# Kernel optimization log

Hardware: AMD Instinct MI355X
Metric: run time of the kernel (lower is better)

Reference implementation:

```python
import jax, jax.numpy as jnp
import numpy as np

T, B, OBS, H, GH = 512, 256, 512, 256, 256  # time, batch, obs_dim, FC_DIM_SIZE(=GRU hidden), GRU_HIDDEN_DIM (actor width)
ADIMS = (32, 32, 16, 64)
BIG = 1e10


def setup_inputs():
    key = jax.random.key(0)
    ks = jax.random.split(key, 16)
    f = lambda i, shp: (jax.random.normal(ks[i], shp, jnp.float32) / np.float32(np.sqrt(shp[0])))
    inp = {
        "hidden": jnp.zeros((B, H), jnp.float32),
        "obs": jax.random.normal(ks[0], (T, B, OBS), jnp.float32),
        "dones": jax.random.randint(ks[1], (T, B), 0, 2).astype(jnp.int32),
        "avail_lc1": jax.random.randint(ks[2], (T, B, ADIMS[0]), 0, 2).astype(jnp.int32),
        "avail_lc2": jax.random.randint(ks[3], (T, B, ADIMS[1]), 0, 2).astype(jnp.int32),
        "avail_mc": jax.random.randint(ks[4], (T, B, ADIMS[2]), 0, 2).astype(jnp.int32),
        "avail_hint": jax.random.randint(ks[5], (T, B, ADIMS[3]), 0, 2).astype(jnp.int32),
        "W_emb": f(6, (OBS, H)), "b_emb": jnp.zeros((H,), jnp.float32),
        "Wi": f(7, (H, 3 * H)), "bi": jnp.zeros((3 * H,), jnp.float32),
        "Wh": f(8, (H, 3 * H)), "bhn": jnp.zeros((H,), jnp.float32),
        "W_a": f(9, (H, GH)), "b_a": jnp.zeros((GH,), jnp.float32),
        "W_lc1": f(10, (GH, ADIMS[0])), "b_lc1": jnp.zeros((ADIMS[0],), jnp.float32),
        "W_lc2": f(11, (GH, ADIMS[1])), "b_lc2": jnp.zeros((ADIMS[1],), jnp.float32),
        "W_mc": f(12, (GH, ADIMS[2])), "b_mc": jnp.zeros((ADIMS[2],), jnp.float32),
        "W_hint": f(13, (GH, ADIMS[3])), "b_hint": jnp.zeros((ADIMS[3],), jnp.float32),
        "W_c1": f(14, (H, H)), "b_c1": jnp.zeros((H,), jnp.float32),
        "W_c2": f(15, (H, 1)), "b_c2": jnp.zeros((1,), jnp.float32),
    }
    return inp


def _gru_scan(hidden, emb, dones, Wi, bi, Wh, bhn):
    # flax GRUCell math: r=sig(ir+hr), z=sig(iz+hz), n=tanh(in + r*(hn+bhn)), h'=(1-z)*n + z*h
    def step(h, xt):
        e, d = xt  # e: [B,H], d: [B]
        h = jnp.where(d[:, None] != 0, jnp.zeros_like(h), h)  # per-step reset to zero carry
        gi = e @ Wi + bi   # [B,3H]
        gh = h @ Wh        # [B,3H]
        ir, iz, inn = jnp.split(gi, 3, axis=-1)
        hr, hz, hn = jnp.split(gh, 3, axis=-1)
        r = jax.nn.sigmoid(ir + hr)
        z = jax.nn.sigmoid(iz + hz)
        n = jnp.tanh(inn + r * (hn + bhn))
        nh = (1.0 - z) * n + z * h
        return nh, nh
    return jax.lax.scan(step, hidden, (emb, dones))


def reference(hidden, obs, dones, avail_lc1, avail_lc2, avail_mc, avail_hint,
              W_emb, b_emb, Wi, bi, Wh, bhn, W_a, b_a,
              W_lc1, b_lc1, W_lc2, b_lc2, W_mc, b_mc, W_hint, b_hint,
              W_c1, b_c1, W_c2, b_c2):
    emb = jax.nn.relu(obs @ W_emb + b_emb)                    # [T,B,H]
    hidden, y = _gru_scan(hidden, emb, dones, Wi, bi, Wh, bhn)  # y: [T,B,H]
    a = jax.nn.relu(y @ W_a + b_a)                            # [T,B,GH]
    mask = lambda logits, avail: logits - (1.0 - avail.astype(logits.dtype)) * BIG
    l_lc1 = mask(a @ W_lc1 + b_lc1, avail_lc1)
    l_lc2 = mask(a @ W_lc2 + b_lc2, avail_lc2)
    l_mc = mask(a @ W_mc + b_mc, avail_mc)
    l_hint = mask(a @ W_hint + b_hint, avail_hint)
    c = jax.nn.relu(y @ W_c1 + b_c1)                          # [T,B,H]
    critic = jnp.squeeze(c @ W_c2 + b_c2, axis=-1)            # [T,B]
    return (hidden, l_lc1, l_lc2, l_mc, l_hint, critic)
```

## Files before the change

kernel.cpp:

```cpp
#include <hip/hip_runtime.h>
#include <stdint.h>


typedef short short8 __attribute__((ext_vector_type(8)));
typedef float f32x4  __attribute__((ext_vector_type(4)));

#define T_DIM 512
#define CHUNK 32
#define NCH   16
#define GIPL  ((size_t)33554432)

#define OUT_HID  ((size_t)0)
#define OUT_LC1  ((size_t)65536)
#define OUT_LC2  ((size_t)4259840)
#define OUT_MC   ((size_t)8454144)
#define OUT_HINT ((size_t)10551296)
#define OUT_CRIT ((size_t)18939904)

__device__ __forceinline__ unsigned short f2bf(float f) {
    unsigned u = __float_as_uint(f);
    u += 0x7fffu + ((u >> 16) & 1u);
    return (unsigned short)(u >> 16);
}
__device__ __forceinline__ float bf2f(unsigned short h) {
    return __uint_as_float(((unsigned)h) << 16);
}

__device__ __forceinline__ unsigned short gru_cell(
    float ir, float iz, float inn, float ho,
    float hrv, float hzv, float hnv, float bh)
{
    float rg = 1.f / (1.f + __expf(-(ir + hrv)));
    float z  = 1.f / (1.f + __expf(-(iz + hzv)));
    float ex = __expf(2.f * (inn + rg * (hnv + bh)));
    float n  = 1.f - 2.f / (ex + 1.f);
    return f2bf((1.f - z) * n + z * ho);
}

__global__ __launch_bounds__(256, 4) void k_prep(
    const float* __restrict__ W_emb, const float* __restrict__ Wi,
    const float* __restrict__ Wh,    const float* __restrict__ W_a,
    const float* __restrict__ W_c1,  const float* __restrict__ W_lc1,
    const float* __restrict__ W_lc2, const float* __restrict__ W_mc,
    const float* __restrict__ W_hint,
    const float* __restrict__ b_lc1, const float* __restrict__ b_lc2,
    const float* __restrict__ b_mc,  const float* __restrict__ b_hint,
    unsigned short* __restrict__ WembF, unsigned short* __restrict__ WiF,
    unsigned short* __restrict__ WhF,   unsigned short* __restrict__ WacF,
    unsigned short* __restrict__ WlogF, float* __restrict__ blog,
    int* __restrict__ fixflag)
{
    int i = blockIdx.x * 256 + threadIdx.x;
    if (i < 131072) {
        int jj = i & 7, L = (i >> 3) & 63, kt32 = (i >> 9) & 15;
        int j = (i >> 13) & 3, q = (i >> 15) & 3;
        int n = q * 64 + j * 16 + (L & 15);
        int k = kt32 * 32 + ((L >> 4) << 3) + jj;
        WembF[i] = f2bf(W_emb[k * 256 + n]);
        return;
    }
    i -= 131072;
    if (i < 196608) {
        int jj = i & 7, L = (i >> 3) & 63, kk32 = (i >> 9) & 7;
        int j = (i >> 12) & 3, q = (i >> 14) & 3, nc = i >> 16;
        int n = nc * 256 + q * 64 + j * 16 + (L & 15);
        int k = kk32 * 32 + ((L >> 4) << 3) + jj;
        WiF[i] = f2bf(Wi[k * 768 + n]);
        return;
    }
    i -= 196608;
    if (i < 196608) {
        int jj = i & 7, L = (i >> 3) & 63, ks = (i >> 9) & 7, rest = i >> 12;
        int w = rest / 6, i6 = rest % 6, rho = i6 >> 1, s = i6 & 1;
        int k   = ks * 32 + ((L >> 4) << 3) + jj;
        int col = rho * 256 + w * 32 + s * 16 + (L & 15);
        WhF[i] = f2bf(Wh[k * 768 + col]);
        return;
    }
    i -= 196608;
    if (i < 131072) {
        int jj = i & 7, L = (i >> 3) & 63, kk32 = (i >> 9) & 7;
        int j = (i >> 12) & 3, q = (i >> 14) & 3, nc = (i >> 16) & 1;
        int n = nc * 256 + q * 64 + j * 16 + (L & 15);
        int k = kk32 * 32 + ((L >> 4) << 3) + jj;
        WacF[i] = f2bf(n < 256 ? W_a[k * 256 + n] : W_c1[k * 256 + (n - 256)]);
        return;
    }
    i -= 131072;
    if (i < 40960) {
        int jj = i & 7, L = (i >> 3) & 63, kk32 = (i >> 9) & 7;
        int j = i >> 12;
        int n = j * 16 + (L & 15);
        int k = kk32 * 32 + ((L >> 4) << 3) + jj;
        float v;
        if      (n < 32)  v = W_lc1[k * 32 + n];
        else if (n < 64)  v = W_lc2[k * 32 + (n - 32)];
        else if (n < 80)  v = W_mc [k * 16 + (n - 64)];
        else if (n < 144) v = W_hint[k * 64 + (n - 80)];
        else              v = 0.f;
        WlogF[i] = f2bf(v);
        return;
    }
    i -= 40960;
    if (i < 160) {
        float v;
        if      (i < 32)  v = b_lc1[i];
        else if (i < 64)  v = b_lc2[i - 32];
        else if (i < 80)  v = b_mc [i - 64];
        else if (i < 144) v = b_hint[i - 80];
        else              v = 0.f;
        blog[i] = v;
        return;
    }
    i -= 160;
    if (i == 0) *fixflag = 0;
}

__global__ __launch_bounds__(512, 3) void k_fused_g12(
    const float* __restrict__ obs, const unsigned short* __restrict__ WembF,
    const float* __restrict__ b_emb, const unsigned short* __restrict__ WiF,
    const float* __restrict__ bi, unsigned short* __restrict__ out)
{
    __shared__ unsigned short As[64][72];
    __shared__ unsigned short eS[64][264];
    const int tid = threadIdx.x, w = tid >> 6, L = tid & 63;
    const int mq = (w >> 2) * 32, wq = w & 3, nq = wq * 64;
    const int m0 = blockIdx.x * 64;
    const int lc = L & 15, lq8 = (L >> 4) * 8, lr = (L >> 4) * 4;
    const int sra = tid >> 3, sha = (tid & 7) * 8;

    f32x4 acc[2][4];
#pragma unroll
    for (int i = 0; i < 2; i++)
#pragma unroll
        for (int j = 0; j < 4; j++) acc[i][j] = 0;

    const float* Ag = obs + (size_t)(m0 + sra) * 512 + sha;
    for (int kt = 0; kt < 512; kt += 64) {
        {
            f32x4 v0 = *(const f32x4*)(Ag + kt);
            f32x4 v1 = *(const f32x4*)(Ag + kt + 4);
            short8 pk;
            pk[0] = (short)f2bf(v0[0]); pk[1] = (short)f2bf(v0[1]);
            pk[2] = (short)f2bf(v0[2]); pk[3] = (short)f2bf(v0[3]);
            pk[4] = (short)f2bf(v1[0]); pk[5] = (short)f2bf(v1[1]);
            pk[6] = (short)f2bf(v1[2]); pk[7] = (short)f2bf(v1[3]);
            *(short8*)&As[sra][sha] = pk;
        }
        __syncthreads();
#pragma unroll
        for (int ks = 0; ks < 2; ks++) {
            const int kt32 = (kt >> 5) + ks;
            short8 a[2], b[4];
#pragma unroll
            for (int i = 0; i < 2; i++)
                a[i] = *(const short8*)&As[mq + i * 16 + lc][ks * 32 + lq8];
#pragma unroll
            for (int j = 0; j < 4; j++)
                b[j] = *(const short8*)(WembF +
                        ((((size_t)(wq * 4 + j) * 16 + kt32) * 64 + L) * 8));
#pragma unroll
            for (int i = 0; i < 2; i++)
#pragma unroll
                for (int j = 0; j < 4; j++)
                    acc[i][j] = __builtin_amdgcn_mfma_f32_16x16x32_bf16(a[i], b[j], acc[i][j], 0, 0, 0);
        }
        __syncthreads();
    }
#pragma unroll
    for (int i = 0; i < 2; i++)
#pragma unroll
        for (int j = 0; j < 4; j++) {
            int col = nq + j * 16 + lc;
            float bv = b_emb[col];
#pragma unroll
            for (int rg = 0; rg < 4; rg++) {
                int row = mq + i * 16 + lr + rg;
                eS[row][col] = f2bf(fmaxf(acc[i][j][rg] + bv, 0.f));
            }
        }
    __syncthreads();

    for (int nc = 0; nc < 3; nc++) {
#pragma unroll
        for (int i = 0; i < 2; i++)
#pragma unroll
            for (int j = 0; j < 4; j++) acc[i][j] = 0;

#pragma unroll 2
        for (int kk = 0; kk < 256; kk += 32) {
            const int kk32 = kk >> 5;
            short8 a[2], b[4];
#pragma unroll
            for (int i = 0; i < 2; i++)
                a[i] = *(const short8*)&eS[mq + i * 16 + lc][kk + lq8];
#pragma unroll
            for (int j = 0; j < 4; j++)
                b[j] = *(const short8*)(WiF +
                        ((((size_t)((nc * 4 + wq) * 4 + j) * 8 + kk32) * 64 + L) * 8));
#pragma unroll
            for (int i = 0; i < 2; i++)
#pragma unroll
                for (int j = 0; j < 4; j++)
                    acc[i][j] = __builtin_amdgcn_mfma_f32_16x16x32_bf16(a[i], b[j], acc[i][j], 0, 0, 0);
        }
#pragma unroll
        for (int i = 0; i < 2; i++) {
            const int row0  = m0 + mq + i * 16 + lr;
            const int t     = row0 >> 8;
            const int g     = (row0 >> 4) & 15;
            const int rowg2 = (row0 >> 2) & 3;
#pragma unroll
            for (int jh = 0; jh < 2; jh++) {
                const int colb = nc * 256 + nq + jh * 32;
                const int gate = colb >> 8;
                const int w2   = (colb & 255) >> 5;
                short8 pk;
#pragma unroll
                for (int rg = 0; rg < 4; rg++)
#pragma unroll
                    for (int s = 0; s < 2; s++) {
                        int col = colb + s * 16 + lc;
                        float v = acc[i][jh * 2 + s][rg] + bi[col];
                        pk[rg * 2 + s] = (short)f2bf(v);
                    }
                size_t dst = (size_t)gate * GIPL +
                             (((size_t)(t * 16 + g) * 512) + (size_t)w2 * 64 +
                              (size_t)rowg2 * 16 + lc) * 8;
                *(short8*)(out + dst) = pk;
            }
        }
    }
}

__global__ __launch_bounds__(512, 3) void k_gemm_ac(
    const unsigned short* __restrict__ y, const unsigned short* __restrict__ WacF,
    const float* __restrict__ b_a, const float* __restrict__ b_c1,
    unsigned short* __restrict__ out)
{
    __shared__ unsigned short yS[64][264];
    const int tid = threadIdx.x, w = tid >> 6, L = tid & 63;
    const int mq = (w >> 2) * 32, wq = w & 3, nq = wq * 64;
    const int m0 = blockIdx.x * 64;
    const int lc = L & 15, lq8 = (L >> 4) * 8, lr = (L >> 4) * 4;

    {
        int r = tid >> 3, cb = (tid & 7) * 32;
        const unsigned short* yg = y + (size_t)(m0 + r) * 256 + cb;
#pragma unroll
        for (int c = 0; c < 32; c += 8)
            *(short8*)&yS[r][cb + c] = *(const short8*)(yg + c);
    }
    __syncthreads();

    for (int nc = 0; nc < 2; nc++) {
        f32x4 acc[2][4];
#pragma unroll
        for (int i = 0; i < 2; i++)
#pragma unroll
            for (int j = 0; j < 4; j++) acc[i][j] = 0;

#pragma unroll 2
        for (int kk = 0; kk < 256; kk += 32) {
            const int kk32 = kk >> 5;
            short8 a[2], b[4];
#pragma unroll
            for (int i = 0; i < 2; i++)
                a[i] = *(const short8*)&yS[mq + i * 16 + lc][kk + lq8];
#pragma unroll
            for (int j = 0; j < 4; j++)
                b[j] = *(const short8*)(WacF +
                        ((((size_t)((nc * 4 + wq) * 4 + j) * 8 + kk32) * 64 + L) * 8));
#pragma unroll
            for (int i = 0; i < 2; i++)
#pragma unroll
                for (int j = 0; j < 4; j++)
                    acc[i][j] = __builtin_amdgcn_mfma_f32_16x16x32_bf16(a[i], b[j], acc[i][j], 0, 0, 0);
        }
#pragma unroll
        for (int i = 0; i < 2; i++)
#pragma unroll
            for (int j = 0; j < 4; j++) {
                int col = nc * 256 + nq + j * 16 + lc;
                float bv = (col < 256) ? b_a[col] : b_c1[col - 256];
#pragma unroll
                for (int rg = 0; rg < 4; rg++) {
                    int row = m0 + mq + i * 16 + lr + rg;
                    out[(size_t)row * 512 + col] = f2bf(fmaxf(acc[i][j][rg] + bv, 0.f));
                }
            }
    }
}

__global__ __launch_bounds__(512, 1) void k_gru_main(
    const unsigned short* __restrict__ gi, const unsigned short* __restrict__ WhF,
    const int* __restrict__ dones, const float* __restrict__ h0,
    const float* __restrict__ bhn, unsigned short* __restrict__ y,
    unsigned short* __restrict__ hend)
{
    __shared__ unsigned short hT[2][16][264];
    __shared__ unsigned short yS[2][16][256];
    __shared__ unsigned int rowbits[16];
    const int tid = threadIdx.x, w = tid >> 6, L = tid & 63;
    const int g = blockIdx.x & 15, c = blockIdx.x >> 4;
    const int b0 = g * 16, t0 = c * CHUNK;
    const int rowg = L >> 4, lc = L & 15;

    short8 Bf[6][8];
#pragma unroll
    for (int i6 = 0; i6 < 6; i6++)
#pragma unroll
        for (int ks = 0; ks < 8; ks++)
            Bf[i6][ks] = *(const short8*)(WhF + ((((size_t)w * 6 + i6) * 8 + ks) * 64 + L) * 8);

    const float bh0 = bhn[w * 32 + lc], bh1 = bhn[w * 32 + 16 + lc];

    if (tid < 16) rowbits[tid] = 0;
    __syncthreads();
    {
        int tp = tid >> 4, r = tid & 15;
        if (dones[(t0 + tp) * 256 + b0 + r]) atomicOr(&rowbits[r], 1u << tp);
    }
    __syncthreads();

    unsigned rbr[4];
#pragma unroll
    for (int r = 0; r < 4; r++) rbr[r] = rowbits[rowg * 4 + r];

    {
        int hrow = tid >> 5, hcol = (tid & 31) * 8;
        bool rz = (rowbits[hrow] & 1u) != 0;
#pragma unroll
        for (int cc = 0; cc < 8; cc++) {
            unsigned short v = 0;
            if (c == 0 && !rz) v = f2bf(h0[(b0 + hrow) * 256 + hcol + cc]);
            hT[0][hrow][hcol + cc] = v;
        }
    }
    __syncthreads();

    const size_t gstep = (size_t)16 * 512 * 8;
    size_t gb = ((size_t)(t0 * 16 + g) * 512 + tid) * 8;
    short8 vir = *(const short8*)(gi + gb);
    short8 viz = *(const short8*)(gi + GIPL + gb);
    short8 vin = *(const short8*)(gi + 2 * GIPL + gb);

#pragma unroll 2
    for (int tp = 0; tp < CHUNK; tp++) {
        const int cur = tp & 1, nxt = cur ^ 1;
        const int t = t0 + tp;

        short8 nir, niz, nin;
        if (tp + 1 < CHUNK) {
            size_t gn = gb + (size_t)(tp + 1) * gstep;
            nir = *(const short8*)(gi + gn);
            niz = *(const short8*)(gi + GIPL + gn);
            nin = *(const short8*)(gi + 2 * GIPL + gn);
        }

        f32x4 acc0 = 0, acc1 = 0, acc2 = 0, acc3 = 0, acc4 = 0, acc5 = 0;
#pragma unroll
        for (int ks = 0; ks < 8; ks++) {
            short8 a = *(const short8*)&hT[cur][lc][ks * 32 + rowg * 8];
            acc0 = __builtin_amdgcn_mfma_f32_16x16x32_bf16(a, Bf[0][ks], acc0, 0, 0, 0);
            acc1 = __builtin_amdgcn_mfma_f32_16x16x32_bf16(a, Bf[1][ks], acc1, 0, 0, 0);
            acc2 = __builtin_amdgcn_mfma_f32_16x16x32_bf16(a, Bf[2][ks], acc2, 0, 0, 0);
            acc3 = __builtin_amdgcn_mfma_f32_16x16x32_bf16(a, Bf[3][ks], acc3, 0, 0, 0);
            acc4 = __builtin_amdgcn_mfma_f32_16x16x32_bf16(a, Bf[4][ks], acc4, 0, 0, 0);
            acc5 = __builtin_amdgcn_mfma_f32_16x16x32_bf16(a, Bf[5][ks], acc5, 0, 0, 0);
        }

#pragma unroll
        for (int s = 0; s < 2; s++) {
            const int j = w * 32 + s * 16 + lc;
            f32x4 hrv = s ? acc1 : acc0;
            f32x4 hzv = s ? acc3 : acc2;
            f32x4 hnv = s ? acc5 : acc4;
            float bh = s ? bh1 : bh0;
#pragma unroll
            for (int r = 0; r < 4; r++) {
                int row = rowg * 4 + r;
                float ir  = bf2f((unsigned short)vir[r * 2 + s]);
                float iz  = bf2f((unsigned short)viz[r * 2 + s]);
                float inn = bf2f((unsigned short)vin[r * 2 + s]);
                float ho  = bf2f(hT[cur][row][j]);
                unsigned short hb = gru_cell(ir, iz, inn, ho, hrv[r], hzv[r], hnv[r], bh);
                yS[cur][row][j] = hb;
                unsigned short hw = hb;
                if (tp + 1 < CHUNK && ((rbr[r] >> (tp + 1)) & 1u)) hw = 0;
                hT[nxt][row][j] = hw;
            }
        }
        __syncthreads();

        {
            int yrow = tid >> 5, ycol = (tid & 31) * 8;
            short8 yv = *(const short8*)&yS[cur][yrow][ycol];
            *(short8*)(y + ((size_t)t * 256 + b0 + yrow) * 256 + ycol) = yv;
            if (tp == CHUNK - 1)
                *(short8*)(hend + ((size_t)c * 256 + b0 + yrow) * 256 + ycol) = yv;
        }

        vir = nir; viz = niz; vin = nin;
    }
}

__global__ __launch_bounds__(512, 1) void k_gru_fix_par(
    const unsigned short* __restrict__ gi, const unsigned short* __restrict__ WhF,
    const int* __restrict__ dones, const float* __restrict__ bhn,
    const unsigned short* __restrict__ hend, unsigned short* __restrict__ y,
    int* __restrict__ flag)
{
    __shared__ unsigned short hT[2][16][264];
    __shared__ unsigned int rowbits[16], prevbits[16];
    __shared__ int sh_fd[16];
    const int tid = threadIdx.x, w = tid >> 6, L = tid & 63;
    const int g = blockIdx.x & 15, c = (blockIdx.x >> 4) + 1;
    const int b0 = g * 16, t0 = c * CHUNK;
    const int rowg = L >> 4, lc = L & 15;
    const int hrow = tid >> 5, hcol = (tid & 31) * 8;

    short8 Bf[6][8];
#pragma unroll
    for (int i6 = 0; i6 < 6; i6++)
#pragma unroll
        for (int ks = 0; ks < 8; ks++)
            Bf[i6][ks] = *(const short8*)(WhF + ((((size_t)w * 6 + i6) * 8 + ks) * 64 + L) * 8);

    const float bh0 = bhn[w * 32 + lc], bh1 = bhn[w * 32 + 16 + lc];

    if (tid < 16) { rowbits[tid] = 0; prevbits[tid] = 0; }
    __syncthreads();
    {
        int tp = tid >> 4, r = tid & 15;
        if (dones[(t0 + tp) * 256 + b0 + r])         atomicOr(&rowbits[r],  1u << tp);
        if (dones[(t0 - CHUNK + tp) * 256 + b0 + r]) atomicOr(&prevbits[r], 1u << tp);
    }
    __syncthreads();
    if (tid < 16) {
        unsigned m = rowbits[tid];
        sh_fd[tid] = m ? __builtin_ctz(m) : CHUNK;
        if (prevbits[tid] == 0) atomicOr(flag, 1);
    }
    __syncthreads();

    int maxfix = 0;
    unsigned rbr[4]; int fdr[4];
#pragma unroll
    for (int r = 0; r < 16; r++) maxfix = max(maxfix, sh_fd[r]);
    if (maxfix == 0) return;
#pragma unroll
    for (int r = 0; r < 4; r++) {
        rbr[r] = rowbits[rowg * 4 + r];
        fdr[r] = sh_fd[rowg * 4 + r];
    }

    {
        short8 hv = *(const short8*)(hend + ((size_t)(c - 1) * 256 + b0 + hrow) * 256 + hcol);
        if (rowbits[hrow] & 1u) { short8 z = {0,0,0,0,0,0,0,0}; hv = z; }
        *(short8*)&hT[0][hrow][hcol] = hv;
    }
    __syncthreads();

    const size_t gstep = (size_t)16 * 512 * 8;
    const size_t gb0 = ((size_t)(t0 * 16 + g) * 512 + tid) * 8;

    int cur = 0;
    for (int tp = 0; tp < maxfix; tp++) {
        const int nxt = cur ^ 1;

        f32x4 acc0 = 0, acc1 = 0, acc2 = 0, acc3 = 0, acc4 = 0, acc5 = 0;
#pragma unroll
        for (int ks = 0; ks < 8; ks++) {
            short8 a = *(const short8*)&hT[cur][lc][ks * 32 + rowg * 8];
            acc0 = __builtin_amdgcn_mfma_f32_16x16x32_bf16(a, Bf[0][ks], acc0, 0, 0, 0);
            acc1 = __builtin_amdgcn_mfma_f32_16x16x32_bf16(a, Bf[1][ks], acc1, 0, 0, 0);
            acc2 = __builtin_amdgcn_mfma_f32_16x16x32_bf16(a, Bf[2][ks], acc2, 0, 0, 0);
            acc3 = __builtin_amdgcn_mfma_f32_16x16x32_bf16(a, Bf[3][ks], acc3, 0, 0, 0);
            acc4 = __builtin_amdgcn_mfma_f32_16x16x32_bf16(a, Bf[4][ks], acc4, 0, 0, 0);
            acc5 = __builtin_amdgcn_mfma_f32_16x16x32_bf16(a, Bf[5][ks], acc5, 0, 0, 0);
        }

        size_t gb = gb0 + (size_t)tp * gstep;
        short8 vir = *(const short8*)(gi + gb);
        short8 viz = *(const short8*)(gi + GIPL + gb);
        short8 vin = *(const short8*)(gi + 2 * GIPL + gb);

        unsigned short* yb = y + (size_t)((t0 + tp) * 256 + b0) * 256;
#pragma unroll
        for (int s = 0; s < 2; s++) {
            const int j = w * 32 + s * 16 + lc;
            f32x4 hrv = s ? acc1 : acc0;
            f32x4 hzv = s ? acc3 : acc2;
            f32x4 hnv = s ? acc5 : acc4;
            float bh = s ? bh1 : bh0;
#pragma unroll
            for (int r = 0; r < 4; r++) {
                int row = rowg * 4 + r;
                float ir  = bf2f((unsigned short)vir[r * 2 + s]);
                float iz  = bf2f((unsigned short)viz[r * 2 + s]);
                float inn = bf2f((unsigned short)vin[r * 2 + s]);
                float ho  = bf2f(hT[cur][row][j]);
                unsigned short hb = gru_cell(ir, iz, inn, ho, hrv[r], hzv[r], hnv[r], bh);
                if (tp < fdr[r]) yb[row * 256 + j] = hb;
                unsigned short hw = hb;
                if (tp + 1 < CHUNK && ((rbr[r] >> (tp + 1)) & 1u)) hw = 0;
                hT[nxt][row][j] = hw;
            }
        }
        __syncthreads();
        cur = nxt;
    }
}

__global__ __launch_bounds__(512, 1) void k_gru_fix(
    const unsigned short* __restrict__ gi, const unsigned short* __restrict__ WhF,
    const int* __restrict__ dones, const float* __restrict__ bhn,
    const unsigned short* __restrict__ hend, unsigned short* __restrict__ y,
    const int* __restrict__ flag)
{
    if (*flag == 0) return;

    __shared__ unsigned short hT[2][16][264];
    __shared__ unsigned int rowbits[16];
    __shared__ int sh_fd[16];
    const int tid = threadIdx.x, w = tid >> 6, L = tid & 63;
    const int b0 = blockIdx.x * 16, g = blockIdx.x;
    const int rowg = L >> 4, lc = L & 15;
    const int hrow = tid >> 5, hcol = (tid & 31) * 8;

    short8 Bf[6][8];
#pragma unroll
    for (int i6 = 0; i6 < 6; i6++)
#pragma unroll
        for (int ks = 0; ks < 8; ks++)
            Bf[i6][ks] = *(const short8*)(WhF + ((((size_t)w * 6 + i6) * 8 + ks) * 64 + L) * 8);

    const float bh0 = bhn[w * 32 + lc], bh1 = bhn[w * 32 + 16 + lc];

    *(short8*)&hT[0][hrow][hcol] =
        *(const short8*)(hend + (size_t)(b0 + hrow) * 256 + hcol);
    int cur = 0;

    const size_t gstep = (size_t)16 * 512 * 8;

    for (int c = 1; c < NCH; c++) {
        const int t0 = c * CHUNK;
        if (tid < 16) rowbits[tid] = 0;
        __syncthreads();
        {
            int tp = tid >> 4, r = tid & 15;
            if (dones[(t0 + tp) * 256 + b0 + r]) atomicOr(&rowbits[r], 1u << tp);
        }
        __syncthreads();
        if (tid < 16) {
            unsigned m = rowbits[tid];
            sh_fd[tid] = m ? __builtin_ctz(m) : CHUNK;
        }
        __syncthreads();

        int maxfix = 0;
        unsigned rbr[4]; int fdr[4];
#pragma unroll
        for (int r = 0; r < 16; r++) maxfix = max(maxfix, sh_fd[r]);
#pragma unroll
        for (int r = 0; r < 4; r++) {
            rbr[r] = rowbits[rowg * 4 + r];
            fdr[r] = sh_fd[rowg * 4 + r];
        }
        if (rowbits[hrow] & 1u) {
#pragma unroll
            for (int cc = 0; cc < 8; cc++) hT[cur][hrow][hcol + cc] = 0;
        }
        __syncthreads();

        const size_t gb0 = ((size_t)(t0 * 16 + g) * 512 + tid) * 8;

        for (int tp = 0; tp < maxfix; tp++) {
            const int nxt = cur ^ 1;

            f32x4 acc0 = 0, acc1 = 0, acc2 = 0, acc3 = 0, acc4 = 0, acc5 = 0;
#pragma unroll
            for (int ks = 0; ks < 8; ks++) {
                short8 a = *(const short8*)&hT[cur][lc][ks * 32 + rowg * 8];
                acc0 = __builtin_amdgcn_mfma_f32_16x16x32_bf16(a, Bf[0][ks], acc0, 0, 0, 0);
                acc1 = __builtin_amdgcn_mfma_f32_16x16x32_bf16(a, Bf[1][ks], acc1, 0, 0, 0);
                acc2 = __builtin_amdgcn_mfma_f32_16x16x32_bf16(a, Bf[2][ks], acc2, 0, 0, 0);
                acc3 = __builtin_amdgcn_mfma_f32_16x16x32_bf16(a, Bf[3][ks], acc3, 0, 0, 0);
                acc4 = __builtin_amdgcn_mfma_f32_16x16x32_bf16(a, Bf[4][ks], acc4, 0, 0, 0);
                acc5 = __builtin_amdgcn_mfma_f32_16x16x32_bf16(a, Bf[5][ks], acc5, 0, 0, 0);
            }

            size_t gb = gb0 + (size_t)tp * gstep;
            short8 vir = *(const short8*)(gi + gb);
            short8 viz = *(const short8*)(gi + GIPL + gb);
            short8 vin = *(const short8*)(gi + 2 * GIPL + gb);

            unsigned short* yb = y + (size_t)((t0 + tp) * 256 + b0) * 256;
#pragma unroll
            for (int s = 0; s < 2; s++) {
                const int j = w * 32 + s * 16 + lc;
                f32x4 hrv = s ? acc1 : acc0;
                f32x4 hzv = s ? acc3 : acc2;
                f32x4 hnv = s ? acc5 : acc4;
                float bh = s ? bh1 : bh0;
#pragma unroll
                for (int r = 0; r < 4; r++) {
                    int row = rowg * 4 + r;
                    float ir  = bf2f((unsigned short)vir[r * 2 + s]);
                    float iz  = bf2f((unsigned short)viz[r * 2 + s]);
                    float inn = bf2f((unsigned short)vin[r * 2 + s]);
                    float ho  = bf2f(hT[cur][row][j]);
                    unsigned short hb = gru_cell(ir, iz, inn, ho, hrv[r], hzv[r], hnv[r], bh);
                    if (tp < fdr[r]) yb[row * 256 + j] = hb;
                    unsigned short hw = hb;
                    if (tp + 1 < CHUNK && ((rbr[r] >> (tp + 1)) & 1u)) hw = 0;
                    hT[nxt][row][j] = hw;
                }
            }
            __syncthreads();
            cur = nxt;
        }

        if (sh_fd[hrow] < CHUNK) {
            *(short8*)&hT[cur][hrow][hcol] =
                *(const short8*)(hend + ((size_t)c * 256 + b0 + hrow) * 256 + hcol);
        }
        __syncthreads();
    }
}

__global__ __launch_bounds__(256, 2) void k_logits(
    const unsigned short* __restrict__ ac, const unsigned short* __restrict__ WlogF,
    const float* __restrict__ blog,
    const int* __restrict__ av1, const int* __restrict__ av2,
    const int* __restrict__ av3, const int* __restrict__ av4,
    float* __restrict__ outp)
{
    __shared__ unsigned short As[128][72];
    const int tid = threadIdx.x, w = tid >> 6, L = tid & 63;
    const int m0 = blockIdx.x * 128;
    const int sr = tid >> 1, sh = (tid & 1) * 32;
    const int lc = L & 15, lq8 = (L >> 4) * 8, lr = (L >> 4) * 4;

    f32x4 acc[2][10];
#pragma unroll
    for (int i = 0; i < 2; i++)
#pragma unroll
        for (int j = 0; j < 10; j++) acc[i][j] = 0;

    const unsigned short* Ag = ac + (size_t)(m0 + sr) * 512 + sh;

    for (int kt = 0; kt < 256; kt += 64) {
#pragma unroll
        for (int c = 0; c < 32; c += 8)
            *(short8*)&As[sr][sh + c] = *(const short8*)(Ag + kt + c);
        __syncthreads();
#pragma unroll
        for (int ks = 0; ks < 2; ks++) {
            const int kk32 = (kt >> 5) + ks;
            short8 a[2], b[10];
#pragma unroll
            for (int i = 0; i < 2; i++)
                a[i] = *(const short8*)&As[w * 32 + i * 16 + lc][ks * 32 + lq8];
#pragma unroll
            for (int j = 0; j < 10; j++)
                b[j] = *(const short8*)(WlogF + ((((size_t)j * 8 + kk32) * 64 + L) * 8));
#pragma unroll
            for (int i = 0; i < 2; i++)
#pragma unroll
                for (int j = 0; j < 10; j++)
                    acc[i][j] = __builtin_amdgcn_mfma_f32_16x16x32_bf16(a[i], b[j], acc[i][j], 0, 0, 0);
        }
        __syncthreads();
    }
#pragma unroll
    for (int j = 0; j < 10; j++) {
        int col = j * 16 + lc;
        if (col >= 144) continue;
        int gbase, adim; const int* av; size_t obase;
        if      (col < 32) { gbase = 0;  adim = 32; av = av1; obase = OUT_LC1; }
        else if (col < 64) { gbase = 32; adim = 32; av = av2; obase = OUT_LC2; }
        else if (col < 80) { gbase = 64; adim = 16; av = av3; obase = OUT_MC;  }
        else               { gbase = 80; adim = 64; av = av4; obase = OUT_HINT;}
        int cof = col - gbase;
        float bv = blog[col];
#pragma unroll
        for (int i = 0; i < 2; i++)
#pragma unroll
            for (int rg = 0; rg < 4; rg++) {
                int R = m0 + w * 32 + i * 16 + lr + rg;
                float v = acc[i][j][rg] + bv;
                int a_ = av[(size_t)R * adim + cof];
                v -= (1.f - (float)a_) * 1e10f;
                outp[obase + (size_t)R * adim + cof] = v;
            }
    }
}

__global__ __launch_bounds__(256, 4) void k_critic(
    const unsigned short* __restrict__ ac, const float* __restrict__ W_c2,
    const float* __restrict__ b_c2, float* __restrict__ outp)
{
    const int tid = threadIdx.x, w = tid >> 6, L = tid & 63;
    f32x4 wv = *(const f32x4*)(W_c2 + L * 4);
    float bb = b_c2[0];
    int base = blockIdx.x * 64 + w * 16;
    for (int rr = 0; rr < 16; rr++) {
        int R = base + rr;
        const unsigned short* p = ac + (size_t)R * 512 + 256 + L * 4;
        float s = bf2f(p[0]) * wv[0] + bf2f(p[1]) * wv[1] +
                  bf2f(p[2]) * wv[2] + bf2f(p[3]) * wv[3];
#pragma unroll
        for (int o = 32; o > 0; o >>= 1) s += __shfl_down(s, o);
        if (L == 0) outp[OUT_CRIT + R] = s + bb;
    }
}

__global__ __launch_bounds__(256, 4) void k_hidden(
    const unsigned short* __restrict__ y, float* __restrict__ outp)
{
    int i = blockIdx.x * 256 + threadIdx.x;
    outp[OUT_HID + i] = bf2f(y[(size_t)511 * 65536 + i]);
}

extern "C" void kernel_launch(void* const* d_in, const int* in_sizes, int n_in,
                              void* d_out, int out_size, void* d_ws, size_t ws_size,
                              hipStream_t stream)
{
    const float* hidden = (const float*)d_in[0];
    const float* obs    = (const float*)d_in[1];
    const int*   dones  = (const int*)d_in[2];
    const int*   av1    = (const int*)d_in[3];
    const int*   av2    = (const int*)d_in[4];
    const int*   av3    = (const int*)d_in[5];
    const int*   av4    = (const int*)d_in[6];
    const float* W_emb  = (const float*)d_in[7];
    const float* b_emb  = (const float*)d_in[8];
    const float* Wi     = (const float*)d_in[9];
    const float* bi     = (const float*)d_in[10];
    const float* Wh     = (const float*)d_in[11];
    const float* bhn    = (const float*)d_in[12];
    const float* W_a    = (const float*)d_in[13];
    const float* b_a    = (const float*)d_in[14];
    const float* W_lc1  = (const float*)d_in[15];
    const float* b_lc1  = (const float*)d_in[16];
    const float* W_lc2  = (const float*)d_in[17];
    const float* b_lc2  = (const float*)d_in[18];
    const float* W_mc   = (const float*)d_in[19];
    const float* b_mc   = (const float*)d_in[20];
    const float* W_hint = (const float*)d_in[21];
    const float* b_hint = (const float*)d_in[22];
    const float* W_c1   = (const float*)d_in[23];
    const float* b_c1   = (const float*)d_in[24];
    const float* W_c2   = (const float*)d_in[25];
    const float* b_c2   = (const float*)d_in[26];

    char* ws = (char*)d_ws;
    unsigned short* WembF = (unsigned short*)(ws + 0);
    unsigned short* WiF   = (unsigned short*)(ws + 262144);
    unsigned short* WhF   = (unsigned short*)(ws + 655360);
    unsigned short* WacF  = (unsigned short*)(ws + 1048576);
    unsigned short* WlogF = (unsigned short*)(ws + 1310720);
    float*          blog  = (float*)(ws + 1392640);
    int*            fflag = (int*)(ws + 1393280);
    unsigned short* hend  = (unsigned short*)(ws + 1393664);
    unsigned short* ac    = hend;
    unsigned short* gibuf = (unsigned short*)(ws + 135611392);
    unsigned short* ybuf  = (unsigned short*)(ws + 336937984);
    float* outp = (float*)d_out;

    k_prep<<<2721, 256, 0, stream>>>(W_emb, Wi, Wh, W_a, W_c1, W_lc1, W_lc2,
                                     W_mc, W_hint, b_lc1, b_lc2, b_mc, b_hint,
                                     WembF, WiF, WhF, WacF, WlogF, blog, fflag);
    k_fused_g12<<<2048, 512, 0, stream>>>(obs, WembF, b_emb, WiF, bi, gibuf);
    k_gru_main<<<256, 512, 0, stream>>>(gibuf, WhF, dones, hidden, bhn, ybuf, hend);
    k_gru_fix_par<<<240, 512, 0, stream>>>(gibuf, WhF, dones, bhn, hend, ybuf, fflag);
    k_gru_fix<<<16, 512, 0, stream>>>(gibuf, WhF, dones, bhn, hend, ybuf, fflag);
    k_gemm_ac<<<2048, 512, 0, stream>>>(ybuf, WacF, b_a, b_c1, ac);
    k_logits<<<1024, 256, 0, stream>>>(ac, WlogF, blog, av1, av2, av3, av4, outp);
    k_critic<<<2048, 256, 0, stream>>>(ac, W_c2, b_c2, outp);
    k_hidden<<<2048 / 8, 256, 0, stream>>>(ybuf, outp);
}
```

Baseline: 873.6 us.

## Fuse actor/critic GEMM, logits, critic head and hidden copy into one kernel

Replaces the separate actor/critic GEMM, logits, critic-reduction and final-hidden kernels with a single k_head kernel. Actor and critic activations stay in shared memory instead of round-tripping a 64 MB bf16 buffer through global memory, and three kernel launches go away. The embedding GEMM also double-buffers its A tile so the next obs slice is converted and staged while the current one feeds the MFMAs, leaving one barrier per iteration. The cost is more registers (two accumulator sets) and more LDS per block, with launch bounds lowered from 3 to 2 blocks per CU, which may reduce occupancy.

Result: no change. 858.4 us (-1.7%).

```diff
diff --git a/kernel.cpp b/kernel.cpp
--- a/kernel.cpp
+++ b/kernel.cpp
@@ -121,7 +121,7 @@
     const float* __restrict__ b_emb, const unsigned short* __restrict__ WiF,
     const float* __restrict__ bi, unsigned short* __restrict__ out)
 {
-    __shared__ unsigned short As[64][72];
+    __shared__ unsigned short As[2][64][72];
     __shared__ unsigned short eS[64][264];
     const int tid = threadIdx.x, w = tid >> 6, L = tid & 63;
     const int mq = (w >> 2) * 32, wq = w & 3, nq = wq * 64;
@@ -129,32 +129,37 @@
     const int lc = L & 15, lq8 = (L >> 4) * 8, lr = (L >> 4) * 4;
     const int sra = tid >> 3, sha = (tid & 7) * 8;
 
+    const float* Ag = obs + (size_t)(m0 + sra) * 512 + sha;
+
+    auto stage_a = [&](int kt, int p) {
+        f32x4 v0 = *(const f32x4*)(Ag + kt);
+        f32x4 v1 = *(const f32x4*)(Ag + kt + 4);
+        short8 pk;
+        pk[0] = (short)f2bf(v0[0]); pk[1] = (short)f2bf(v0[1]);
+        pk[2] = (short)f2bf(v0[2]); pk[3] = (short)f2bf(v0[3]);
+        pk[4] = (short)f2bf(v1[0]); pk[5] = (short)f2bf(v1[1]);
+        pk[6] = (short)f2bf(v1[2]); pk[7] = (short)f2bf(v1[3]);
+        *(short8*)&As[p][sra][sha] = pk;
+    };
+
     f32x4 acc[2][4];
 #pragma unroll
     for (int i = 0; i < 2; i++)
 #pragma unroll
         for (int j = 0; j < 4; j++) acc[i][j] = 0;
 
-    const float* Ag = obs + (size_t)(m0 + sra) * 512 + sha;
+    stage_a(0, 0);
+    __syncthreads();
+    int p = 0;
     for (int kt = 0; kt < 512; kt += 64) {
-        {
-            f32x4 v0 = *(const f32x4*)(Ag + kt);
-            f32x4 v1 = *(const f32x4*)(Ag + kt + 4);
-            short8 pk;
-            pk[0] = (short)f2bf(v0[0]); pk[1] = (short)f2bf(v0[1]);
-            pk[2] = (short)f2bf(v0[2]); pk[3] = (short)f2bf(v0[3]);
-            pk[4] = (short)f2bf(v1[0]); pk[5] = (short)f2bf(v1[1]);
-            pk[6] = (short)f2bf(v1[2]); pk[7] = (short)f2bf(v1[3]);
-            *(short8*)&As[sra][sha] = pk;
-        }
-        __syncthreads();
+        if (kt + 64 < 512) stage_a(kt + 64, p ^ 1);
 #pragma unroll
         for (int ks = 0; ks < 2; ks++) {
             const int kt32 = (kt >> 5) + ks;
             short8 a[2], b[4];
 #pragma unroll
             for (int i = 0; i < 2; i++)
-                a[i] = *(const short8*)&As[mq + i * 16 + lc][ks * 32 + lq8];
+                a[i] = *(const short8*)&As[p][mq + i * 16 + lc][ks * 32 + lq8];
 #pragma unroll
             for (int j = 0; j < 4; j++)
                 b[j] = *(const short8*)(WembF +
@@ -166,6 +171,7 @@
                     acc[i][j] = __builtin_amdgcn_mfma_f32_16x16x32_bf16(a[i], b[j], acc[i][j], 0, 0, 0);
         }
         __syncthreads();
+        p ^= 1;
     }
 #pragma unroll
     for (int i = 0; i < 2; i++)
@@ -233,12 +239,17 @@
     }
 }
 
-__global__ __launch_bounds__(512, 3) void k_gemm_ac(
+__global__ __launch_bounds__(512, 2) void k_head(
     const unsigned short* __restrict__ y, const unsigned short* __restrict__ WacF,
     const float* __restrict__ b_a, const float* __restrict__ b_c1,
-    unsigned short* __restrict__ out)
+    const unsigned short* __restrict__ WlogF, const float* __restrict__ blog,
+    const float* __restrict__ W_c2, const float* __restrict__ b_c2,
+    const int* __restrict__ av1, const int* __restrict__ av2,
+    const int* __restrict__ av3, const int* __restrict__ av4,
+    float* __restrict__ outp)
 {
     __shared__ unsigned short yS[64][264];
+    __shared__ unsigned short aS[64][264];
     const int tid = threadIdx.x, w = tid >> 6, L = tid & 63;
     const int mq = (w >> 2) * 32, wq = w & 3, nq = wq * 64;
     const int m0 = blockIdx.x * 64;
@@ -253,42 +264,109 @@
     }
     __syncthreads();
 
-    for (int nc = 0; nc < 2; nc++) {
-        f32x4 acc[2][4];
+    if (m0 >= 130816) {
+        int r = tid >> 3, cb = (tid & 7) * 32;
+        int b = (m0 - 130816) + r;
+#pragma unroll
+        for (int c = 0; c < 32; c++)
+            outp[OUT_HID + (size_t)b * 256 + cb + c] = bf2f(yS[r][cb + c]);
+    }
+
+    f32x4 accA[2][4], accC[2][4];
+#pragma unroll
+    for (int i = 0; i < 2; i++)
+#pragma unroll
+        for (int j = 0; j < 4; j++) { accA[i][j] = 0; accC[i][j] = 0; }
+
+#pragma unroll 2
+    for (int kk32 = 0; kk32 < 8; kk32++) {
+        short8 a[2], bA[4], bC[4];
 #pragma unroll
         for (int i = 0; i < 2; i++)
-#pragma unroll
-            for (int j = 0; j < 4; j++) acc[i][j] = 0;
+            a[i] = *(const short8*)&yS[mq + i * 16 + lc][kk32 * 32 + lq8];
+#pragma unroll
+        for (int j = 0; j < 4; j++) {
+            bA[j] = *(const short8*)(WacF +
+                    ((((size_t)(wq * 4 + j) * 8 + kk32) * 64 + L) * 8));
+            bC[j] = *(const short8*)(WacF +
+                    ((((size_t)((4 + wq) * 4 + j) * 8 + kk32) * 64 + L) * 8));
+        }
+#pragma unroll
+        for (int i = 0; i < 2; i++)
+#pragma unroll
+            for (int j = 0; j < 4; j++) {
+                accA[i][j] = __builtin_amdgcn_mfma_f32_16x16x32_bf16(a[i], bA[j], accA[i][j], 0, 0, 0);
+                accC[i][j] = __builtin_amdgcn_mfma_f32_16x16x32_bf16(a[i], bC[j], accC[i][j], 0, 0, 0);
+            }
+    }
+    __syncthreads();
+
+#pragma unroll
+    for (int i = 0; i < 2; i++)
+#pragma unroll
+        for (int j = 0; j < 4; j++) {
+            int col = nq + j * 16 + lc;
+            float bvA = b_a[col], bvC = b_c1[col];
+#pragma unroll
+            for (int rg = 0; rg < 4; rg++) {
+                int row = mq + i * 16 + lr + rg;
+                aS[row][col] = f2bf(fmaxf(accA[i][j][rg] + bvA, 0.f));
+                yS[row][col] = f2bf(fmaxf(accC[i][j][rg] + bvC, 0.f));
+            }
+        }
+    __syncthreads();
+
+    {
+        const int mf = w >> 1, jh = (w & 1) * 5;
+        f32x4 accL[5];
+#pragma unroll
+        for (int j5 = 0; j5 < 5; j5++) accL[j5] = 0;
 
 #pragma unroll 2
-        for (int kk = 0; kk < 256; kk += 32) {
-            const int kk32 = kk >> 5;
-            short8 a[2], b[4];
-#pragma unroll
-            for (int i = 0; i < 2; i++)
-                a[i] = *(const short8*)&yS[mq + i * 16 + lc][kk + lq8];
-#pragma unroll
-            for (int j = 0; j < 4; j++)
-                b[j] = *(const short8*)(WacF +
-                        ((((size_t)((nc * 4 + wq) * 4 + j) * 8 + kk32) * 64 + L) * 8));
-#pragma unroll
-            for (int i = 0; i < 2; i++)
-#pragma unroll
-                for (int j = 0; j < 4; j++)
-                    acc[i][j] = __builtin_amdgcn_mfma_f32_16x16x32_bf16(a[i], b[j], acc[i][j], 0, 0, 0);
-        }
-#pragma unroll
-        for (int i = 0; i < 2; i++)
-#pragma unroll
-            for (int j = 0; j < 4; j++) {
-                int col = nc * 256 + nq + j * 16 + lc;
-                float bv = (col < 256) ? b_a[col] : b_c1[col - 256];
-#pragma unroll
-                for (int rg = 0; rg < 4; rg++) {
-                    int row = m0 + mq + i * 16 + lr + rg;
-                    out[(size_t)row * 512 + col] = f2bf(fmaxf(acc[i][j][rg] + bv, 0.f));
-                }
-            }
+        for (int kk32 = 0; kk32 < 8; kk32++) {
+            short8 a = *(const short8*)&aS[mf * 16 + lc][kk32 * 32 + lq8];
+#pragma unroll
+            for (int j5 = 0; j5 < 5; j5++) {
+                short8 b = *(const short8*)(WlogF +
+                        ((((size_t)(jh + j5) * 8 + kk32) * 64 + L) * 8));
+                accL[j5] = __builtin_amdgcn_mfma_f32_16x16x32_bf16(a, b, accL[j5], 0, 0, 0);
+            }
+        }
+#pragma unroll
+        for (int j5 = 0; j5 < 5; j5++) {
+            int col = (jh + j5) * 16 + lc;
+            if (col >= 144) continue;
+            int gbase, adim; const int* av; size_t obase;
+            if      (col < 32) { gbase = 0;  adim = 32; av = av1; obase = OUT_LC1; }
+            else if (col < 64) { gbase = 32; adim = 32; av = av2; obase = OUT_LC2; }
+            else if (col < 80) { gbase = 64; adim = 16; av = av3; obase = OUT_MC;  }
+            else               { gbase = 80; adim = 64; av = av4; obase = OUT_HINT;}
+            int cof = col - gbase;
+            float bv = blog[col];
+#pragma unroll
+            for (int rg = 0; rg < 4; rg++) {
+                int R = m0 + mf * 16 + lr + rg;
+                float v = accL[j5][rg] + bv;
+                int a_ = av[(size_t)R * adim + cof];
+                v -= (1.f - (float)a_) * 1e10f;
+                outp[obase + (size_t)R * adim + cof] = v;
+            }
+        }
+    }
+
+    {
+        f32x4 wv = *(const f32x4*)(W_c2 + L * 4);
+        float bb = b_c2[0];
+#pragma unroll
+        for (int rr = 0; rr < 8; rr++) {
+            int row = w * 8 + rr;
+            const unsigned short* pc = &yS[row][L * 4];
+            float s = bf2f(pc[0]) * wv[0] + bf2f(pc[1]) * wv[1] +
+                      bf2f(pc[2]) * wv[2] + bf2f(pc[3]) * wv[3];
+#pragma unroll
+            for (int o = 32; o > 0; o >>= 1) s += __shfl_down(s, o);
+            if (L == 0) outp[OUT_CRIT + m0 + row] = s + bb;
+        }
     }
 }
 
@@ -628,100 +706,6 @@
         }
         __syncthreads();
     }
-}
-
-__global__ __launch_bounds__(256, 2) void k_logits(
-    const unsigned short* __restrict__ ac, const unsigned short* __restrict__ WlogF,
-    const float* __restrict__ blog,
-    const int* __restrict__ av1, const int* __restrict__ av2,
-    const int* __restrict__ av3, const int* __restrict__ av4,
-    float* __restrict__ outp)
-{
-    __shared__ unsigned short As[128][72];
-    const int tid = threadIdx.x, w = tid >> 6, L = tid & 63;
-    const int m0 = blockIdx.x * 128;
-    const int sr = tid >> 1, sh = (tid & 1) * 32;
-    const int lc = L & 15, lq8 = (L >> 4) * 8, lr = (L >> 4) * 4;
-
-    f32x4 acc[2][10];
-#pragma unroll
-    for (int i = 0; i < 2; i++)
-#pragma unroll
-        for (int j = 0; j < 10; j++) acc[i][j] = 0;
-
-    const unsigned short* Ag = ac + (size_t)(m0 + sr) * 512 + sh;
-
-    for (int kt = 0; kt < 256; kt += 64) {
-#pragma unroll
-        for (int c = 0; c < 32; c += 8)
-            *(short8*)&As[sr][sh + c] = *(const short8*)(Ag + kt + c);
-        __syncthreads();
-#pragma unroll
-        for (int ks = 0; ks < 2; ks++) {
-            const int kk32 = (kt >> 5) + ks;
-            short8 a[2], b[10];
-#pragma unroll
-            for (int i = 0; i < 2; i++)
-                a[i] = *(const short8*)&As[w * 32 + i * 16 + lc][ks * 32 + lq8];
-#pragma unroll
-            for (int j = 0; j < 10; j++)
-                b[j] = *(const short8*)(WlogF + ((((size_t)j * 8 + kk32) * 64 + L) * 8));
-#pragma unroll
-            for (int i = 0; i < 2; i++)
-#pragma unroll
-                for (int j = 0; j < 10; j++)
-                    acc[i][j] = __builtin_amdgcn_mfma_f32_16x16x32_bf16(a[i], b[j], acc[i][j], 0, 0, 0);
-        }
-        __syncthreads();
-    }
-#pragma unroll
-    for (int j = 0; j < 10; j++) {
-        int col = j * 16 + lc;
-        if (col >= 144) continue;
-        int gbase, adim; const int* av; size_t obase;
-        if      (col < 32) { gbase = 0;  adim = 32; av = av1; obase = OUT_LC1; }
-        else if (col < 64) { gbase = 32; adim = 32; av = av2; obase = OUT_LC2; }
-        else if (col < 80) { gbase = 64; adim = 16; av = av3; obase = OUT_MC;  }
-        else               { gbase = 80; adim = 64; av = av4; obase = OUT_HINT;}
-        int cof = col - gbase;
-        float bv = blog[col];
-#pragma unroll
-        for (int i = 0; i < 2; i++)
-#pragma unroll
-            for (int rg = 0; rg < 4; rg++) {
-                int R = m0 + w * 32 + i * 16 + lr + rg;
-                float v = acc[i][j][rg] + bv;
-                int a_ = av[(size_t)R * adim + cof];
-                v -= (1.f - (float)a_) * 1e10f;
-                outp[obase + (size_t)R * adim + cof] = v;
-            }
-    }
-}
-
-__global__ __launch_bounds__(256, 4) void k_critic(
-    const unsigned short* __restrict__ ac, const float* __restrict__ W_c2,
-    const float* __restrict__ b_c2, float* __restrict__ outp)
-{
-    const int tid = threadIdx.x, w = tid >> 6, L = tid & 63;
-    f32x4 wv = *(const f32x4*)(W_c2 + L * 4);
-    float bb = b_c2[0];
-    int base = blockIdx.x * 64 + w * 16;
-    for (int rr = 0; rr < 16; rr++) {
-        int R = base + rr;
-        const unsigned short* p = ac + (size_t)R * 512 + 256 + L * 4;
-        float s = bf2f(p[0]) * wv[0] + bf2f(p[1]) * wv[1] +
-                  bf2f(p[2]) * wv[2] + bf2f(p[3]) * wv[3];
-#pragma unroll
-        for (int o = 32; o > 0; o >>= 1) s += __shfl_down(s, o);
-        if (L == 0) outp[OUT_CRIT + R] = s + bb;
-    }
-}
-
-__global__ __launch_bounds__(256, 4) void k_hidden(
-    const unsigned short* __restrict__ y, float* __restrict__ outp)
-{
-    int i = blockIdx.x * 256 + threadIdx.x;
-    outp[OUT_HID + i] = bf2f(y[(size_t)511 * 65536 + i]);
 }
 
 extern "C" void kernel_launch(void* const* d_in, const int* in_sizes, int n_in,
@@ -765,7 +749,6 @@
     float*          blog  = (float*)(ws + 1392640);
     int*            fflag = (int*)(ws + 1393280);
     unsigned short* hend  = (unsigned short*)(ws + 1393664);
-    unsigned short* ac    = hend;
     unsigned short* gibuf = (unsigned short*)(ws + 135611392);
     unsigned short* ybuf  = (unsigned short*)(ws + 336937984);
     float* outp = (float*)d_out;
@@ -777,8 +760,6 @@
     k_gru_main<<<256, 512, 0, stream>>>(gibuf, WhF, dones, hidden, bhn, ybuf, hend);
     k_gru_fix_par<<<240, 512, 0, stream>>>(gibuf, WhF, dones, bhn, hend, ybuf, fflag);
     k_gru_fix<<<16, 512, 0, stream>>>(gibuf, WhF, dones, bhn, hend, ybuf, fflag);
-    k_gemm_ac<<<2048, 512, 0, stream>>>(ybuf, WacF, b_a, b_c1, ac);
-    k_logits<<<1024, 256, 0, stream>>>(ac, WlogF, blog, av1, av2, av3, av4, outp);
-    k_critic<<<2048, 256, 0, stream>>>(ac, W_c2, b_c2, outp);
-    k_hidden<<<2048 / 8, 256, 0, stream>>>(ybuf, outp);
-}
+    k_head<<<2048, 512, 0, stream>>>(ybuf, WacF, b_a, b_c1, WlogF, blog,
+                                     W_c2, b_c2, av1, av2, av3, av4, outp);
+}
```
